# Optimization experiments

Measured on AMD Instinct MI355X. Metric: run time of the kernel, lower is better.

Reference implementation:

```python
import jax, jax.numpy as jnp
import numpy as np

D_IN = 1024
D_OUT = 1024
NUM_HEADS = 16
HEAD_DIM = D_OUT // NUM_HEADS


def setup_inputs() -> dict:
    key = jax.random.key(0)
    ks = jax.random.split(key, 6)
    s = 0.02
    x = jax.random.normal(ks[0], (2, 2048, D_IN), dtype=jnp.float32)
    Wq = jax.random.normal(ks[1], (D_IN, D_OUT), dtype=jnp.float32) * s
    Wk = jax.random.normal(ks[2], (D_IN, D_OUT), dtype=jnp.float32) * s
    Wv = jax.random.normal(ks[3], (D_IN, D_OUT), dtype=jnp.float32) * s
    Wo = jax.random.normal(ks[4], (D_OUT, D_OUT), dtype=jnp.float32) * s
    bo = jnp.zeros((D_OUT,), dtype=jnp.float32)
    return {"x": x, "Wq": Wq, "Wk": Wk, "Wv": Wv, "Wo": Wo, "bo": bo}


def reference(x, Wq, Wk, Wv, Wo, bo):
    b, n, _ = x.shape
    # project and split heads: [b, h, n, d]
    def heads(W):
        return (x @ W).reshape(b, n, NUM_HEADS, HEAD_DIM).transpose(0, 2, 1, 3)
    q, k, v = heads(Wq), heads(Wk), heads(Wv)
    scores = jnp.einsum("bhqd,bhkd->bhqk", q, k)  # [b,h,n,n]
    causal = jnp.tril(jnp.ones((n, n), dtype=bool))  # True = keep
    scores = jnp.where(causal, scores, -jnp.inf)
    attn = jax.nn.softmax(scores / np.sqrt(HEAD_DIM).astype(np.float32), axis=-1)
    ctx = jnp.einsum("bhqk,bhkd->bhqd", attn, v)
    ctx = ctx.transpose(0, 2, 1, 3).reshape(b, n, D_OUT)
    return ctx @ Wo + bo
```

## Files before the change

kernel.cpp:

```cpp
#include <hip/hip_runtime.h>
#include <stdint.h>

typedef unsigned short u16;
typedef __attribute__((ext_vector_type(8))) __bf16 bf16x8;
typedef __attribute__((ext_vector_type(4))) float f32x4;
typedef __attribute__((ext_vector_type(16))) float f32x16;

#define D_IN 1024
#define NH 16
#define DH 64
#define BATCH 2
#define SEQ 2048

#define QSCL 0.1803368801111244f

#define GLD_LDS16(gp, lp)                                                              \
  __builtin_amdgcn_global_load_lds((__attribute__((address_space(1))) const void*)(gp), \
                                   (__attribute__((address_space(3))) void*)(lp), 16, 0, 0)

__device__ __forceinline__ u16 f2b(float f) {
  union { float ff; uint32_t u; } v; v.ff = f;
  return (u16)((v.u + 0x7fffu + ((v.u >> 16) & 1u)) >> 16);
}

__device__ __forceinline__ float swap32f(float v) { return __shfl_xor(v, 32, 64); }

__device__ __forceinline__ uint32_t cvtpk(float a, float b) {
  uint32_t r;
  asm("v_cvt_pk_bf16_f32 %0, %1, %2" : "=v"(r) : "v"(a), "v"(b));
  return r;
}
__device__ __forceinline__ float fexp2(float x) {
  float r;
  asm("v_exp_f32 %0, %1" : "=v"(r) : "v"(x));
  return r;
}

__global__ __launch_bounds__(256)
void prep_kernel(const float* __restrict__ x, u16* __restrict__ xb,
                 const float* __restrict__ W0, const float* __restrict__ W1,
                 const float* __restrict__ W2, const float* __restrict__ W3,
                 u16* __restrict__ T0, u16* __restrict__ T1,
                 u16* __restrict__ T2, u16* __restrict__ T3) {
  __shared__ float tile[32][33];
  if (blockIdx.x < 4096) {
    const int i = (blockIdx.x * 256 + threadIdx.x) * 4;
    const float4 v = *(const float4*)(x + i);
    uint2 pack;
    pack.x = (uint32_t)f2b(v.x) | ((uint32_t)f2b(v.y) << 16);
    pack.y = (uint32_t)f2b(v.z) | ((uint32_t)f2b(v.w) << 16);
    *(uint2*)(xb + i) = pack;
  } else {
    const int bid2 = blockIdx.x - 4096;
    const float* W; u16* T;
    switch (bid2 >> 10) {
      case 0: W = W0; T = T0; break;
      case 1: W = W1; T = T1; break;
      case 2: W = W2; T = T2; break;
      default: W = W3; T = T3; break;
    }
    const int rem = bid2 & 1023;
    const int n0 = (rem >> 5) * 32, k0 = (rem & 31) * 32;
    const int tx = threadIdx.x & 31, ty = threadIdx.x >> 5;
    #pragma unroll
    for (int i = 0; i < 32; i += 8)
      tile[ty + i][tx] = W[(size_t)(k0 + ty + i) * D_IN + n0 + tx];
    __syncthreads();
    #pragma unroll
    for (int i = 0; i < 32; i += 8)
      T[(size_t)(n0 + ty + i) * D_IN + k0 + tx] = f2b(tile[tx][ty + i]);
  }
}

__device__ __forceinline__ void qkv_compute(
    const u16* __restrict__ AsB, const u16* __restrict__ Bq,
    const u16* __restrict__ Bk, const u16* __restrict__ Bv,
    int wm, int wn, int g, int lm,
    f32x4 accq[4][2], f32x4 acck[4][2], f32x4 accv[4][2]) {
  #pragma unroll
  for (int kk = 0; kk < 2; ++kk) {
    const int slot = ((kk * 4 + g) ^ (lm & 7)) << 3;
    bf16x8 af[4];
    #pragma unroll
    for (int i = 0; i < 4; ++i)
      af[i] = *(const bf16x8*)(AsB + (wm * 64 + i * 16 + lm) * 64 + slot);
    bf16x8 bq[2], bk[2], bv[2];
    #pragma unroll
    for (int n = 0; n < 2; ++n) {
      const int ro = (wn * 32 + n * 16 + lm) * 64 + slot;
      bq[n] = *(const bf16x8*)(Bq + ro);
      bk[n] = *(const bf16x8*)(Bk + ro);
      bv[n] = *(const bf16x8*)(Bv + ro);
    }
    #pragma unroll
    for (int i = 0; i < 4; ++i)
      #pragma unroll
      for (int n = 0; n < 2; ++n) {
        accq[i][n] = __builtin_amdgcn_mfma_f32_16x16x32_bf16(af[i], bq[n], accq[i][n], 0, 0, 0);
        acck[i][n] = __builtin_amdgcn_mfma_f32_16x16x32_bf16(af[i], bk[n], acck[i][n], 0, 0, 0);
        accv[i][n] = __builtin_amdgcn_mfma_f32_16x16x32_bf16(af[i], bv[n], accv[i][n], 0, 0, 0);
      }
  }
}

__global__ __launch_bounds__(512)
void gemm_qkv_kernel(const u16* __restrict__ Xb,
                     const u16* __restrict__ WqT, const u16* __restrict__ WkT,
                     const u16* __restrict__ WvT,
                     u16* __restrict__ Qo, u16* __restrict__ Ko, u16* __restrict__ Vt) {
  __shared__ u16 As[2][128 * 64];
  __shared__ u16 Bs[2][3][128 * 64];

  const int tid = threadIdx.x;
  const int lane = tid & 63;
  const int w = tid >> 6;
  const int wm = w >> 2, wn = w & 3;
  const int bm = blockIdx.x * 128;
  const int bn = blockIdx.y * 128;
  const int g = lane >> 4, lm = lane & 15;

  const int r_in = lane >> 3;
  const int s_w = lane & 7;
  const int swz_col = (s_w ^ r_in) << 3;

  const int c0 = w * 2;
  const u16* a_src0 = Xb + (size_t)(bm + c0 * 8 + r_in) * D_IN + swz_col;
  const u16* a_src1 = a_src0 + 8 * D_IN;
  const u16* q_src0 = WqT + (size_t)(bn + c0 * 8 + r_in) * D_IN + swz_col;
  const u16* q_src1 = q_src0 + 8 * D_IN;
  const u16* k_src0 = WkT + (size_t)(bn + c0 * 8 + r_in) * D_IN + swz_col;
  const u16* k_src1 = k_src0 + 8 * D_IN;
  const u16* v_src0 = WvT + (size_t)(bn + c0 * 8 + r_in) * D_IN + swz_col;
  const u16* v_src1 = v_src0 + 8 * D_IN;

#define QKV_STAGE(BUF, K0)                                 \
  do {                                                     \
    GLD_LDS16(a_src0 + (K0), &As[BUF][c0 * 512]);          \
    GLD_LDS16(a_src1 + (K0), &As[BUF][c0 * 512 + 512]);    \
    GLD_LDS16(q_src0 + (K0), &Bs[BUF][0][c0 * 512]);       \
    GLD_LDS16(q_src1 + (K0), &Bs[BUF][0][c0 * 512 + 512]); \
    GLD_LDS16(k_src0 + (K0), &Bs[BUF][1][c0 * 512]);       \
    GLD_LDS16(k_src1 + (K0), &Bs[BUF][1][c0 * 512 + 512]); \
    GLD_LDS16(v_src0 + (K0), &Bs[BUF][2][c0 * 512]);       \
    GLD_LDS16(v_src1 + (K0), &Bs[BUF][2][c0 * 512 + 512]); \
  } while (0)

  f32x4 accq[4][2], acck[4][2], accv[4][2];
  #pragma unroll
  for (int i = 0; i < 4; ++i)
    #pragma unroll
    for (int n = 0; n < 2; ++n) {
      accq[i][n] = {0.f, 0.f, 0.f, 0.f};
      acck[i][n] = {0.f, 0.f, 0.f, 0.f};
      accv[i][n] = {0.f, 0.f, 0.f, 0.f};
    }

  QKV_STAGE(0, 0);
  QKV_STAGE(1, 64);
  #pragma unroll 1
  for (int tt = 0; tt < 7; ++tt) {
    asm volatile("s_waitcnt vmcnt(8)" ::: "memory");
    __builtin_amdgcn_s_barrier();
    qkv_compute(As[0], Bs[0][0], Bs[0][1], Bs[0][2], wm, wn, g, lm, accq, acck, accv);
    __builtin_amdgcn_s_barrier();
    QKV_STAGE(0, (2 * tt + 2) * 64);
    asm volatile("s_waitcnt vmcnt(8)" ::: "memory");
    __builtin_amdgcn_s_barrier();
    qkv_compute(As[1], Bs[1][0], Bs[1][1], Bs[1][2], wm, wn, g, lm, accq, acck, accv);
    __builtin_amdgcn_s_barrier();
    QKV_STAGE(1, (2 * tt + 3) * 64);
  }
  asm volatile("s_waitcnt vmcnt(8)" ::: "memory");
  __builtin_amdgcn_s_barrier();
  qkv_compute(As[0], Bs[0][0], Bs[0][1], Bs[0][2], wm, wn, g, lm, accq, acck, accv);
  asm volatile("s_waitcnt vmcnt(0)" ::: "memory");
  __builtin_amdgcn_s_barrier();
  qkv_compute(As[1], Bs[1][0], Bs[1][1], Bs[1][2], wm, wn, g, lm, accq, acck, accv);
#undef QKV_STAGE

  #pragma unroll
  for (int i = 0; i < 4; ++i) {
    #pragma unroll
    for (int n = 0; n < 2; ++n) {
      #pragma unroll
      for (int r = 0; r < 4; ++r) {
        const int m = bm + wm * 64 + i * 16 + g * 4 + r;
        const int c = bn + wn * 32 + n * 16 + lm;
        const int b = m >> 11, nn = m & (SEQ - 1);
        const int h = c >> 6, d = c & (DH - 1);
        const int bh = b * NH + h;
        const int t = nn >> 5;
        {
          const u16 val = f2b(accq[i][n][r] * QSCL);
          const int st = d >> 4;
          const int lane2 = ((d >> 3) & 1) * 32 + (nn & 31);
          const int j = d & 7;
          Qo[((size_t)(bh * 64 + t) * 4 + st) * 512 + lane2 * 8 + j] = val;
        }
        {
          const u16 val = f2b(acck[i][n][r]);
          const int st = d >> 4;
          const int lane2 = ((d >> 3) & 1) * 32 + (nn & 31);
          const int j = d & 7;
          Ko[((size_t)(bh * 64 + t) * 4 + st) * 512 + lane2 * 8 + j] = val;
        }
        {
          const u16 val = f2b(accv[i][n][r]);
          const int n5 = nn & 31;
          const int f = (n5 >> 4) * 2 + (d >> 5);
          const int lane2 = ((n5 >> 2) & 1) * 32 + (d & 31);
          const int j = ((n5 >> 3) & 1) * 4 + (n5 & 3);
          Vt[((size_t)(bh * 64 + t) * 4 + f) * 512 + lane2 * 8 + j] = val;
        }
      }
    }
  }
}

__global__ __launch_bounds__(256)
void attn4_kernel(const u16* __restrict__ Qb, const u16* __restrict__ Kb,
                  const u16* __restrict__ Vt, u16* __restrict__ Ctx) {
  __shared__ float mbuf[4][32][64];
  __shared__ float lbuf[4][32];

  const int tid = threadIdx.x;
  const int lane = tid & 63;
  const int kw = tid >> 6;
  const int ql = lane & 31;
  const int hi = lane >> 5;
  const int bid = blockIdx.x;
  const int c = bid & 7;
  const int r = bid >> 3;
  const int jj = r & 31;
  const int bh = c + 8 * (r >> 5);
  const int b = bh >> 4, h = bh & 15;

  const u16* Qf = Qb + (size_t)bh * 64 * 2048;
  const u16* Kf = Kb + (size_t)bh * 64 * 2048;
  const u16* Vf = Vt + (size_t)bh * 64 * 2048;
  const int lofs = lane * 8;

  #pragma unroll 1
  for (int pass = 0; pass < 2; ++pass) {
    const int qt = pass ? (63 - jj) : jj;
    const int qb0 = qt * 32;

    bf16x8 qf[4];
    {
      const u16* qp = Qf + (size_t)qt * 2048 + lofs;
      #pragma unroll
      for (int st = 0; st < 4; ++st) qf[st] = *(const bf16x8*)(qp + st * 512);
    }

    f32x16 ctx0 = {0,0,0,0,0,0,0,0,0,0,0,0,0,0,0,0};
    f32x16 ctx1 = {0,0,0,0,0,0,0,0,0,0,0,0,0,0,0,0};
    float lacc[4] = {0.f, 0.f, 0.f, 0.f};

    bf16x8 kf[4], vf[4];
    if (kw <= qt) {
      {
        const u16* kp = Kf + (size_t)kw * 2048 + lofs;
        const u16* vp = Vf + (size_t)kw * 2048 + lofs;
        #pragma unroll
        for (int st = 0; st < 4; ++st) kf[st] = *(const bf16x8*)(kp + st * 512);
        #pragma unroll
        for (int f = 0; f < 4; ++f) vf[f] = *(const bf16x8*)(vp + f * 512);
      }
      #pragma unroll 2
      for (int t = kw; t <= qt; t += 4) {
        f32x16 s = {0,0,0,0,0,0,0,0,0,0,0,0,0,0,0,0};
        #pragma unroll
        for (int st = 0; st < 4; ++st)
          s = __builtin_amdgcn_mfma_f32_32x32x16_bf16(kf[st], qf[st], s, 0, 0, 0);

        const int tn = (t + 4 <= qt) ? (t + 4) : qt;
        {
          const u16* kp = Kf + (size_t)tn * 2048 + lofs;
          #pragma unroll
          for (int st = 0; st < 4; ++st) kf[st] = *(const bf16x8*)(kp + st * 512);
        }

        float p[16];
        if (t == qt) {
          #pragma unroll
          for (int cr = 0; cr < 16; ++cr) {
            const int kl = ((cr & 3) + 8 * (cr >> 2)) + 4 * hi;
            p[cr] = (kl > ql) ? 0.f : fexp2(s[cr]);
          }
        } else {
          #pragma unroll
          for (int cr = 0; cr < 16; ++cr) p[cr] = fexp2(s[cr]);
        }
        #pragma unroll
        for (int cr = 0; cr < 16; ++cr) lacc[cr & 3] += p[cr];

        #pragma unroll
        for (int ks = 0; ks < 2; ++ks) {
          uint4 pw;
          pw.x = cvtpk(p[ks * 8 + 0], p[ks * 8 + 1]);
          pw.y = cvtpk(p[ks * 8 + 2], p[ks * 8 + 3]);
          pw.z = cvtpk(p[ks * 8 + 4], p[ks * 8 + 5]);
          pw.w = cvtpk(p[ks * 8 + 6], p[ks * 8 + 7]);
          union { uint4 u; bf16x8 v; } pa; pa.u = pw;
          ctx0 = __builtin_amdgcn_mfma_f32_32x32x16_bf16(vf[ks * 2 + 0], pa.v, ctx0, 0, 0, 0);
          ctx1 = __builtin_amdgcn_mfma_f32_32x32x16_bf16(vf[ks * 2 + 1], pa.v, ctx1, 0, 0, 0);
        }

        {
          const u16* vp = Vf + (size_t)tn * 2048 + lofs;
          #pragma unroll
          for (int f = 0; f < 4; ++f) vf[f] = *(const bf16x8*)(vp + f * 512);
        }
      }
    }

    const float lloc = (lacc[0] + lacc[1]) + (lacc[2] + lacc[3]);
    const float lwv = lloc + swap32f(lloc);

    #pragma unroll
    for (int grp = 0; grp < 4; ++grp) {
      const int ch = grp * 2 + hi;
      f32x4 t0 = {ctx0[grp * 4 + 0], ctx0[grp * 4 + 1], ctx0[grp * 4 + 2], ctx0[grp * 4 + 3]};
      f32x4 t1 = {ctx1[grp * 4 + 0], ctx1[grp * 4 + 1], ctx1[grp * 4 + 2], ctx1[grp * 4 + 3]};
      *(f32x4*)&mbuf[kw][ql][(ch ^ ql) * 4 & 63]       = t0;
      *(f32x4*)&mbuf[kw][ql][((ch + 8) ^ ql) * 4 & 63] = t1;
    }
    if (lane < 32) lbuf[kw][ql] = lwv;
    __syncthreads();

    {
      const int ch0 = kw * 4 + hi * 2;
      f32x4 a0 = {0.f, 0.f, 0.f, 0.f}, a1 = {0.f, 0.f, 0.f, 0.f};
      #pragma unroll
      for (int p2 = 0; p2 < 4; ++p2) {
        a0 += *(const f32x4*)&mbuf[p2][ql][(ch0 ^ ql) * 4 & 63];
        a1 += *(const f32x4*)&mbuf[p2][ql][((ch0 + 1) ^ ql) * 4 & 63];
      }
      const float lt = (lbuf[0][ql] + lbuf[1][ql]) + (lbuf[2][ql] + lbuf[3][ql]);
      const float inv = __builtin_amdgcn_rcpf(lt);
      uint4 pw;
      pw.x = cvtpk(a0[0] * inv, a0[1] * inv);
      pw.y = cvtpk(a0[2] * inv, a0[3] * inv);
      pw.z = cvtpk(a1[0] * inv, a1[1] * inv);
      pw.w = cvtpk(a1[2] * inv, a1[3] * inv);
      *(uint4*)(Ctx + (size_t)(b * SEQ + qb0 + ql) * 1024 + h * 64 + kw * 16 + hi * 8) = pw;
    }
    __syncthreads();
  }
}

__device__ __forceinline__ void out_compute(
    const u16* __restrict__ AsB, const u16* __restrict__ BsB,
    int wr, int wc, int g, int lm, f32x4 acc[4][4]) {
  #pragma unroll
  for (int kk = 0; kk < 2; ++kk) {
    const int slot = ((kk * 4 + g) ^ (lm & 7)) << 3;
    bf16x8 af[4], bf[4];
    #pragma unroll
    for (int i = 0; i < 4; ++i)
      af[i] = *(const bf16x8*)(AsB + (wr * 64 + i * 16 + lm) * 64 + slot);
    #pragma unroll
    for (int n = 0; n < 4; ++n)
      bf[n] = *(const bf16x8*)(BsB + (wc * 64 + n * 16 + lm) * 64 + slot);
    #pragma unroll
    for (int i = 0; i < 4; ++i)
      #pragma unroll
      for (int n = 0; n < 4; ++n)
        acc[i][n] = __builtin_amdgcn_mfma_f32_16x16x32_bf16(af[i], bf[n], acc[i][n], 0, 0, 0);
  }
}

__global__ __launch_bounds__(256)
void gemm_out_kernel(const u16* __restrict__ Ctx, const u16* __restrict__ WoT,
                     const float* __restrict__ bo, float* __restrict__ out) {
  __shared__ u16 As[2][128 * 64];
  __shared__ u16 Bs[2][128 * 64];
  const int tid = threadIdx.x;
  const int lane = tid & 63;
  const int w = tid >> 6;
  const int bm = blockIdx.x * 128;
  const int bn = blockIdx.y * 128;
  const int wr = w >> 1, wc = w & 1;
  const int g = lane >> 4, lm = lane & 15;

  const int r_in = lane >> 3;
  const int s_w = lane & 7;
  const int swz_col = (s_w ^ r_in) << 3;

  const int c0 = w * 4;
  const u16* a_src = Ctx + (size_t)(bm + c0 * 8 + r_in) * D_IN + swz_col;
  const u16* b_src = WoT + (size_t)(bn + c0 * 8 + r_in) * D_IN + swz_col;

#define OUT_STAGE(BUF, K0)                                             \
  do {                                                                 \
    _Pragma("unroll")                                                  \
    for (int j = 0; j < 4; ++j) {                                      \
      GLD_LDS16(a_src + j * 8 * D_IN + (K0), &As[BUF][(c0 + j) * 512]); \
      GLD_LDS16(b_src + j * 8 * D_IN + (K0), &Bs[BUF][(c0 + j) * 512]); \
    }                                                                  \
  } while (0)

  f32x4 acc[4][4];
  #pragma unroll
  for (int i = 0; i < 4; ++i)
    #pragma unroll
    for (int n = 0; n < 4; ++n) acc[i][n] = {0.f, 0.f, 0.f, 0.f};

  OUT_STAGE(0, 0);
  OUT_STAGE(1, 64);
  #pragma unroll 1
  for (int tt = 0; tt < 7; ++tt) {
    asm volatile("s_waitcnt vmcnt(8)" ::: "memory");
    __builtin_amdgcn_s_barrier();
    out_compute(As[0], Bs[0], wr, wc, g, lm, acc);
    __builtin_amdgcn_s_barrier();
    OUT_STAGE(0, (2 * tt + 2) * 64);
    asm volatile("s_waitcnt vmcnt(8)" ::: "memory");
    __builtin_amdgcn_s_barrier();
    out_compute(As[1], Bs[1], wr, wc, g, lm, acc);
    __builtin_amdgcn_s_barrier();
    OUT_STAGE(1, (2 * tt + 3) * 64);
  }
  asm volatile("s_waitcnt vmcnt(8)" ::: "memory");
  __builtin_amdgcn_s_barrier();
  out_compute(As[0], Bs[0], wr, wc, g, lm, acc);
  asm volatile("s_waitcnt vmcnt(0)" ::: "memory");
  __builtin_amdgcn_s_barrier();
  out_compute(As[1], Bs[1], wr, wc, g, lm, acc);
#undef OUT_STAGE

  #pragma unroll
  for (int i = 0; i < 4; ++i)
    #pragma unroll
    for (int n = 0; n < 4; ++n)
      #pragma unroll
      for (int r = 0; r < 4; ++r) {
        const int m = bm + wr * 64 + i * 16 + g * 4 + r;
        const int cidx = bn + wc * 64 + n * 16 + lm;
        out[(size_t)m * 1024 + cidx] = acc[i][n][r] + bo[cidx];
      }
}

extern "C" void kernel_launch(void* const* d_in, const int* in_sizes, int n_in,
                              void* d_out, int out_size, void* d_ws, size_t ws_size,
                              hipStream_t stream) {
  (void)in_sizes; (void)n_in; (void)out_size; (void)ws_size;
  const float* x  = (const float*)d_in[0];
  const float* Wq = (const float*)d_in[1];
  const float* Wk = (const float*)d_in[2];
  const float* Wv = (const float*)d_in[3];
  const float* Wo = (const float*)d_in[4];
  const float* bo = (const float*)d_in[5];
  float* out = (float*)d_out;

  char* ws = (char*)d_ws;
  u16* xb  = (u16*)(ws);
  u16* WqT = (u16*)(ws + (8u << 20));
  u16* WkT = (u16*)(ws + (10u << 20));
  u16* WvT = (u16*)(ws + (12u << 20));
  u16* WoT = (u16*)(ws + (14u << 20));
  u16* Qb  = (u16*)(ws + (16u << 20));
  u16* Kb  = (u16*)(ws + (24u << 20));
  u16* Vt  = (u16*)(ws + (32u << 20));
  u16* Ctx = xb;

  prep_kernel<<<dim3(8192), 256, 0, stream>>>(x, xb, Wq, Wk, Wv, Wo, WqT, WkT, WvT, WoT);
  gemm_qkv_kernel<<<dim3(32, 8), 512, 0, stream>>>(xb, WqT, WkT, WvT, Qb, Kb, Vt);
  attn4_kernel<<<dim3(1024), 256, 0, stream>>>(Qb, Kb, Vt, Ctx);
  gemm_out_kernel<<<dim3(32, 8), 256, 0, stream>>>(Ctx, WoT, bo, out);
}
```

Before: 92.65 us.

## Process two adjacent query tiles per attention block to reuse K/V loads

Each attention block now handles two consecutive 32-row query tiles per pass instead of one, so every K and V fragment loaded from global memory feeds both tiles' score and context MFMAs. The grid is halved to 512 blocks and the LDS reduction buffers are doubled to hold both tiles. This cuts K/V global traffic per unit of work, but it raises register pressure with four context accumulators, reduces the block count available for occupancy, and drops the loop unroll to 1.

After: 95.57 us. +3.2%, slower.

```diff
diff --git a/kernel.cpp b/kernel.cpp
--- a/kernel.cpp
+++ b/kernel.cpp
@@ -218,10 +218,10 @@
 }
 
 __global__ __launch_bounds__(256)
-void attn4_kernel(const u16* __restrict__ Qb, const u16* __restrict__ Kb,
+void attn5_kernel(const u16* __restrict__ Qb, const u16* __restrict__ Kb,
                   const u16* __restrict__ Vt, u16* __restrict__ Ctx) {
-  __shared__ float mbuf[4][32][64];
-  __shared__ float lbuf[4][32];
+  __shared__ float mbuf[4][2][32][64];
+  __shared__ float lbuf[4][2][32];
 
   const int tid = threadIdx.x;
   const int lane = tid & 63;
@@ -231,8 +231,8 @@
   const int bid = blockIdx.x;
   const int c = bid & 7;
   const int r = bid >> 3;
-  const int jj = r & 31;
-  const int bh = c + 8 * (r >> 5);
+  const int sp = r & 15;
+  const int bh = c + 8 * (r >> 4);
   const int b = bh >> 4, h = bh & 15;
 
   const u16* Qf = Qb + (size_t)bh * 64 * 2048;
@@ -242,22 +242,29 @@
 
   #pragma unroll 1
   for (int pass = 0; pass < 2; ++pass) {
-    const int qt = pass ? (63 - jj) : jj;
-    const int qb0 = qt * 32;
-
-    bf16x8 qf[4];
+    const int g0 = pass ? (62 - 2 * sp) : (2 * sp);
+    const int g1 = g0 + 1;
+
+    bf16x8 qfA[4], qfB[4];
     {
-      const u16* qp = Qf + (size_t)qt * 2048 + lofs;
-      #pragma unroll
-      for (int st = 0; st < 4; ++st) qf[st] = *(const bf16x8*)(qp + st * 512);
-    }
-
-    f32x16 ctx0 = {0,0,0,0,0,0,0,0,0,0,0,0,0,0,0,0};
-    f32x16 ctx1 = {0,0,0,0,0,0,0,0,0,0,0,0,0,0,0,0};
-    float lacc[4] = {0.f, 0.f, 0.f, 0.f};
+      const u16* qpA = Qf + (size_t)g0 * 2048 + lofs;
+      const u16* qpB = Qf + (size_t)g1 * 2048 + lofs;
+      #pragma unroll
+      for (int st = 0; st < 4; ++st) {
+        qfA[st] = *(const bf16x8*)(qpA + st * 512);
+        qfB[st] = *(const bf16x8*)(qpB + st * 512);
+      }
+    }
+
+    f32x16 cA0 = {0,0,0,0,0,0,0,0,0,0,0,0,0,0,0,0};
+    f32x16 cA1 = {0,0,0,0,0,0,0,0,0,0,0,0,0,0,0,0};
+    f32x16 cB0 = {0,0,0,0,0,0,0,0,0,0,0,0,0,0,0,0};
+    f32x16 cB1 = {0,0,0,0,0,0,0,0,0,0,0,0,0,0,0,0};
+    float lA[4] = {0.f, 0.f, 0.f, 0.f};
+    float lB[4] = {0.f, 0.f, 0.f, 0.f};
 
     bf16x8 kf[4], vf[4];
-    if (kw <= qt) {
+    if (kw <= g1) {
       {
         const u16* kp = Kf + (size_t)kw * 2048 + lofs;
         const u16* vp = Vf + (size_t)kw * 2048 + lofs;
@@ -266,46 +273,82 @@
         #pragma unroll
         for (int f = 0; f < 4; ++f) vf[f] = *(const bf16x8*)(vp + f * 512);
       }
-      #pragma unroll 2
-      for (int t = kw; t <= qt; t += 4) {
-        f32x16 s = {0,0,0,0,0,0,0,0,0,0,0,0,0,0,0,0};
-        #pragma unroll
-        for (int st = 0; st < 4; ++st)
-          s = __builtin_amdgcn_mfma_f32_32x32x16_bf16(kf[st], qf[st], s, 0, 0, 0);
-
-        const int tn = (t + 4 <= qt) ? (t + 4) : qt;
+      #pragma unroll 1
+      for (int t = kw; t <= g1; t += 4) {
+        const int tn = (t + 4 <= g1) ? (t + 4) : g1;
+        const bool doA = (t <= g0);
+
         {
+          f32x16 s = {0,0,0,0,0,0,0,0,0,0,0,0,0,0,0,0};
+          #pragma unroll
+          for (int st = 0; st < 4; ++st)
+            s = __builtin_amdgcn_mfma_f32_32x32x16_bf16(kf[st], qfB[st], s, 0, 0, 0);
+          float p[16];
+          if (t == g1) {
+            #pragma unroll
+            for (int cr = 0; cr < 16; ++cr) {
+              const int kl = ((cr & 3) + 8 * (cr >> 2)) + 4 * hi;
+              p[cr] = (kl > ql) ? 0.f : fexp2(s[cr]);
+            }
+          } else {
+            #pragma unroll
+            for (int cr = 0; cr < 16; ++cr) p[cr] = fexp2(s[cr]);
+          }
+          #pragma unroll
+          for (int cr = 0; cr < 16; ++cr) lB[cr & 3] += p[cr];
+          #pragma unroll
+          for (int ks = 0; ks < 2; ++ks) {
+            uint4 pw;
+            pw.x = cvtpk(p[ks * 8 + 0], p[ks * 8 + 1]);
+            pw.y = cvtpk(p[ks * 8 + 2], p[ks * 8 + 3]);
+            pw.z = cvtpk(p[ks * 8 + 4], p[ks * 8 + 5]);
+            pw.w = cvtpk(p[ks * 8 + 6], p[ks * 8 + 7]);
+            union { uint4 u; bf16x8 v; } pa; pa.u = pw;
+            cB0 = __builtin_amdgcn_mfma_f32_32x32x16_bf16(vf[ks * 2 + 0], pa.v, cB0, 0, 0, 0);
+            cB1 = __builtin_amdgcn_mfma_f32_32x32x16_bf16(vf[ks * 2 + 1], pa.v, cB1, 0, 0, 0);
+          }
+        }
+
+        if (doA) {
+          f32x16 s = {0,0,0,0,0,0,0,0,0,0,0,0,0,0,0,0};
+          #pragma unroll
+          for (int st = 0; st < 4; ++st)
+            s = __builtin_amdgcn_mfma_f32_32x32x16_bf16(kf[st], qfA[st], s, 0, 0, 0);
+          {
+            const u16* kp = Kf + (size_t)tn * 2048 + lofs;
+            #pragma unroll
+            for (int st = 0; st < 4; ++st) kf[st] = *(const bf16x8*)(kp + st * 512);
+          }
+          float p[16];
+          if (t == g0) {
+            #pragma unroll
+            for (int cr = 0; cr < 16; ++cr) {
+              const int kl = ((cr & 3) + 8 * (cr >> 2)) + 4 * hi;
+              p[cr] = (kl > ql) ? 0.f : fexp2(s[cr]);
+            }
+          } else {
+            #pragma unroll
+            for (int cr = 0; cr < 16; ++cr) p[cr] = fexp2(s[cr]);
+          }
+          #pragma unroll
+          for (int cr = 0; cr < 16; ++cr) lA[cr & 3] += p[cr];
+          #pragma unroll
+          for (int ks = 0; ks < 2; ++ks) {
+            uint4 pw;
+            pw.x = cvtpk(p[ks * 8 + 0], p[ks * 8 + 1]);
+            pw.y = cvtpk(p[ks * 8 + 2], p[ks * 8 + 3]);
+            pw.z = cvtpk(p[ks * 8 + 4], p[ks * 8 + 5]);
+            pw.w = cvtpk(p[ks * 8 + 6], p[ks * 8 + 7]);
+            union { uint4 u; bf16x8 v; } pa; pa.u = pw;
+            cA0 = __builtin_amdgcn_mfma_f32_32x32x16_bf16(vf[ks * 2 + 0], pa.v, cA0, 0, 0, 0);
+            cA1 = __builtin_amdgcn_mfma_f32_32x32x16_bf16(vf[ks * 2 + 1], pa.v, cA1, 0, 0, 0);
+          }
+        } else {
           const u16* kp = Kf + (size_t)tn * 2048 + lofs;
           #pragma unroll
           for (int st = 0; st < 4; ++st) kf[st] = *(const bf16x8*)(kp + st * 512);
         }
 
-        float p[16];
-        if (t == qt) {
-          #pragma unroll
-          for (int cr = 0; cr < 16; ++cr) {
-            const int kl = ((cr & 3) + 8 * (cr >> 2)) + 4 * hi;
-            p[cr] = (kl > ql) ? 0.f : fexp2(s[cr]);
-          }
-        } else {
-          #pragma unroll
-          for (int cr = 0; cr < 16; ++cr) p[cr] = fexp2(s[cr]);
-        }
-        #pragma unroll
-        for (int cr = 0; cr < 16; ++cr) lacc[cr & 3] += p[cr];
-
-        #pragma unroll
-        for (int ks = 0; ks < 2; ++ks) {
-          uint4 pw;
-          pw.x = cvtpk(p[ks * 8 + 0], p[ks * 8 + 1]);
-          pw.y = cvtpk(p[ks * 8 + 2], p[ks * 8 + 3]);
-          pw.z = cvtpk(p[ks * 8 + 4], p[ks * 8 + 5]);
-          pw.w = cvtpk(p[ks * 8 + 6], p[ks * 8 + 7]);
-          union { uint4 u; bf16x8 v; } pa; pa.u = pw;
-          ctx0 = __builtin_amdgcn_mfma_f32_32x32x16_bf16(vf[ks * 2 + 0], pa.v, ctx0, 0, 0, 0);
-          ctx1 = __builtin_amdgcn_mfma_f32_32x32x16_bf16(vf[ks * 2 + 1], pa.v, ctx1, 0, 0, 0);
-        }
-
         {
           const u16* vp = Vf + (size_t)tn * 2048 + lofs;
           #pragma unroll
@@ -314,36 +357,49 @@
       }
     }
 
-    const float lloc = (lacc[0] + lacc[1]) + (lacc[2] + lacc[3]);
-    const float lwv = lloc + swap32f(lloc);
-
-    #pragma unroll
-    for (int grp = 0; grp < 4; ++grp) {
-      const int ch = grp * 2 + hi;
-      f32x4 t0 = {ctx0[grp * 4 + 0], ctx0[grp * 4 + 1], ctx0[grp * 4 + 2], ctx0[grp * 4 + 3]};
-      f32x4 t1 = {ctx1[grp * 4 + 0], ctx1[grp * 4 + 1], ctx1[grp * 4 + 2], ctx1[grp * 4 + 3]};
-      *(f32x4*)&mbuf[kw][ql][(ch ^ ql) * 4 & 63]       = t0;
-      *(f32x4*)&mbuf[kw][ql][((ch + 8) ^ ql) * 4 & 63] = t1;
-    }
-    if (lane < 32) lbuf[kw][ql] = lwv;
+    {
+      const float llA = (lA[0] + lA[1]) + (lA[2] + lA[3]);
+      const float lwA = llA + swap32f(llA);
+      const float llB = (lB[0] + lB[1]) + (lB[2] + lB[3]);
+      const float lwB = llB + swap32f(llB);
+      #pragma unroll
+      for (int grp = 0; grp < 4; ++grp) {
+        const int ch = grp * 2 + hi;
+        f32x4 a0 = {cA0[grp * 4 + 0], cA0[grp * 4 + 1], cA0[grp * 4 + 2], cA0[grp * 4 + 3]};
+        f32x4 a1 = {cA1[grp * 4 + 0], cA1[grp * 4 + 1], cA1[grp * 4 + 2], cA1[grp * 4 + 3]};
+        f32x4 b0 = {cB0[grp * 4 + 0], cB0[grp * 4 + 1], cB0[grp * 4 + 2], cB0[grp * 4 + 3]};
+        f32x4 b1 = {cB1[grp * 4 + 0], cB1[grp * 4 + 1], cB1[grp * 4 + 2], cB1[grp * 4 + 3]};
+        *(f32x4*)&mbuf[kw][0][ql][(ch ^ ql) * 4 & 63]       = a0;
+        *(f32x4*)&mbuf[kw][0][ql][((ch + 8) ^ ql) * 4 & 63] = a1;
+        *(f32x4*)&mbuf[kw][1][ql][(ch ^ ql) * 4 & 63]       = b0;
+        *(f32x4*)&mbuf[kw][1][ql][((ch + 8) ^ ql) * 4 & 63] = b1;
+      }
+      if (lane < 32) {
+        lbuf[kw][0][ql] = lwA;
+        lbuf[kw][1][ql] = lwB;
+      }
+    }
     __syncthreads();
 
-    {
+    #pragma unroll
+    for (int sub = 0; sub < 2; ++sub) {
+      const int qt = sub ? g1 : g0;
       const int ch0 = kw * 4 + hi * 2;
       f32x4 a0 = {0.f, 0.f, 0.f, 0.f}, a1 = {0.f, 0.f, 0.f, 0.f};
       #pragma unroll
       for (int p2 = 0; p2 < 4; ++p2) {
-        a0 += *(const f32x4*)&mbuf[p2][ql][(ch0 ^ ql) * 4 & 63];
-        a1 += *(const f32x4*)&mbuf[p2][ql][((ch0 + 1) ^ ql) * 4 & 63];
-      }
-      const float lt = (lbuf[0][ql] + lbuf[1][ql]) + (lbuf[2][ql] + lbuf[3][ql]);
+        a0 += *(const f32x4*)&mbuf[p2][sub][ql][(ch0 ^ ql) * 4 & 63];
+        a1 += *(const f32x4*)&mbuf[p2][sub][ql][((ch0 + 1) ^ ql) * 4 & 63];
+      }
+      const float lt = (lbuf[0][sub][ql] + lbuf[1][sub][ql]) +
+                       (lbuf[2][sub][ql] + lbuf[3][sub][ql]);
       const float inv = __builtin_amdgcn_rcpf(lt);
       uint4 pw;
       pw.x = cvtpk(a0[0] * inv, a0[1] * inv);
       pw.y = cvtpk(a0[2] * inv, a0[3] * inv);
       pw.z = cvtpk(a1[0] * inv, a1[1] * inv);
       pw.w = cvtpk(a1[2] * inv, a1[3] * inv);
-      *(uint4*)(Ctx + (size_t)(b * SEQ + qb0 + ql) * 1024 + h * 64 + kw * 16 + hi * 8) = pw;
+      *(uint4*)(Ctx + (size_t)(b * SEQ + qt * 32 + ql) * 1024 + h * 64 + kw * 16 + hi * 8) = pw;
     }
     __syncthreads();
   }
@@ -391,13 +447,13 @@
   const u16* a_src = Ctx + (size_t)(bm + c0 * 8 + r_in) * D_IN + swz_col;
   const u16* b_src = WoT + (size_t)(bn + c0 * 8 + r_in) * D_IN + swz_col;
 
-#define OUT_STAGE(BUF, K0)                                             \
-  do {                                                                 \
-    _Pragma("unroll")                                                  \
-    for (int j = 0; j < 4; ++j) {                                      \
+#define OUT_STAGE(BUF, K0)                                              \
+  do {                                                                  \
+    _Pragma("unroll")                                                   \
+    for (int j = 0; j < 4; ++j) {                                       \
       GLD_LDS16(a_src + j * 8 * D_IN + (K0), &As[BUF][(c0 + j) * 512]); \
       GLD_LDS16(b_src + j * 8 * D_IN + (K0), &Bs[BUF][(c0 + j) * 512]); \
-    }                                                                  \
+    }                                                                   \
   } while (0)
 
   f32x4 acc[4][4];
@@ -466,6 +522,6 @@
 
   prep_kernel<<<dim3(8192), 256, 0, stream>>>(x, xb, Wq, Wk, Wv, Wo, WqT, WkT, WvT, WoT);
   gemm_qkv_kernel<<<dim3(32, 8), 512, 0, stream>>>(xb, WqT, WkT, WvT, Qb, Kb, Vt);
-  attn4_kernel<<<dim3(1024), 256, 0, stream>>>(Qb, Kb, Vt, Ctx);
+  attn5_kernel<<<dim3(512), 256, 0, stream>>>(Qb, Kb, Vt, Ctx);
   gemm_out_kernel<<<dim3(32, 8), 256, 0, stream>>>(Ctx, WoT, bo, out);
 }
```
